# Performance work log

Hardware: AMD Instinct MI355X
Metric: run time of the kernel (lower is better)

Reference implementation:

```python
import jax, jax.numpy as jnp
import numpy as np

N_NODES = 50000
N_EDGES = 800000
IN_DIM = 128
OUT_DIM = 64
NEG_SLOPE = 0.01  # torch F.leaky_relu default


def setup_inputs() -> dict:
    key = jax.random.key(0)
    ks = jax.random.split(key, 7)
    h = jax.random.normal(ks[0], (N_NODES, IN_DIM), dtype=jnp.float32)
    embed = jax.random.uniform(ks[1], (N_EDGES, 1), dtype=jnp.float32)
    src = jax.random.randint(ks[2], (N_EDGES,), 0, N_NODES)
    dst = jax.random.randint(ks[3], (N_EDGES,), 0, N_NODES)
    # parameters (Linear weights, no bias); stored as [in, out] for x @ W
    W_fc = jax.random.normal(ks[4], (IN_DIM, OUT_DIM), dtype=jnp.float32) / np.sqrt(IN_DIM)
    W_attn = jax.random.normal(ks[5], (3 * OUT_DIM, 1), dtype=jnp.float32) / np.sqrt(3 * OUT_DIM)
    W_feat = jax.random.normal(ks[6], (1, OUT_DIM), dtype=jnp.float32)
    return {"h": h, "embed": embed, "src": src, "dst": dst,
            "W_fc": W_fc, "W_attn": W_attn, "W_feat": W_feat}


def reference(h, embed, src, dst, W_fc, W_attn, W_feat):
    n = h.shape[0]
    z = h @ W_fc                                  # [N, D]
    # split attn weight so we never materialize the [E, 3D] concat
    Wa_src, Wa_dst, Wa_feat = jnp.split(W_attn, 3, axis=0)  # each [D, 1]
    a_src = (z @ Wa_src)[:, 0]                    # [N]
    a_dst = (z @ Wa_dst)[:, 0]                    # [N]
    dfeat = embed @ W_feat                        # [E, D]
    e = a_src[src] + a_dst[dst] + (dfeat @ Wa_feat)[:, 0]  # [E]
    e = jnp.where(e >= 0, e, NEG_SLOPE * e)       # leaky_relu
    # segment softmax over incoming edges of each dst node
    seg_max = jax.ops.segment_max(e, dst, num_segments=n)  # [N]
    ex = jnp.exp(e - seg_max[dst])                # [E]
    denom = jax.ops.segment_sum(ex, dst, num_segments=n)   # [N]
    alpha = ex / denom[dst]                       # [E]
    # weighted scatter-sum of source features
    out = jax.ops.segment_sum(alpha[:, None] * z[src], dst, num_segments=n)  # [N, D]
    return out
```

## Files before the change

### kernel.cpp

```cpp
#include <hip/hip_runtime.h>
#include <hip/hip_fp16.h>

#define N_NODES 50000
#define N_EDGES 800000
#define IN_DIM 128
#define OUT_DIM 64
#define NEG_SLOPE 0.01f

#define BUCK_SHIFT 6
#define BUCK_NODES 64
#define NBUCK ((N_NODES + BUCK_NODES - 1) / BUCK_NODES)
#define CAP 1536
#define EPB 3136
#define NBLK_SCAT ((N_EDGES + EPB - 1) / EPB)

typedef unsigned int uint;

__device__ __forceinline__ uint f2h(float x) {
    return (uint)__half_as_ushort(__float2half_rn(x));
}
__device__ __forceinline__ float h2f(unsigned short u) {
    return __half2float(__ushort_as_half(u));
}

__launch_bounds__(256)
__global__ void k_fc(const float* __restrict__ h,
                     const float* __restrict__ W_fc,
                     const float* __restrict__ W_attn,
                     const float* __restrict__ W_feat,
                     uint* __restrict__ z16, float* __restrict__ a_src, float* __restrict__ a_dst,
                     int* __restrict__ gcursor, float* __restrict__ c_ws) {
    __shared__ float Wlds[IN_DIM * OUT_DIM];
    const float4* Wg = (const float4*)W_fc;
    float4* Wl = (float4*)Wlds;
    #pragma unroll
    for (int i = 0; i < 8; ++i) Wl[threadIdx.x + i * 256] = Wg[threadIdx.x + i * 256];

    int g = blockIdx.x * 256 + threadIdx.x;
    if (g < NBUCK) gcursor[g] = g * CAP;
    if (blockIdx.x == 0 && threadIdx.x < 64) {
        int lane = threadIdx.x;
        float p = W_feat[lane] * W_attn[128 + lane];
        #pragma unroll
        for (int off = 32; off; off >>= 1) p += __shfl_xor(p, off, 64);
        if (lane == 0) c_ws[0] = p;
    }
    __syncthreads();

    int quad = g >> 4;
    int og   = g & 15;
    int n0 = quad * 4;
    if (n0 >= N_NODES) return;

    bool valid[4];
    const float4* hrow[4];
    #pragma unroll
    for (int i = 0; i < 4; ++i) {
        int n = n0 + i;
        valid[i] = (n < N_NODES);
        hrow[i] = (const float4*)(h + (size_t)(valid[i] ? n : (N_NODES - 1)) * IN_DIM);
    }

    float acc[4][4];
    #pragma unroll
    for (int i = 0; i < 4; ++i)
        #pragma unroll
        for (int d = 0; d < 4; ++d) acc[i][d] = 0.f;

    for (int kc = 0; kc < IN_DIM / 4; ++kc) {
        float4 hv[4];
        #pragma unroll
        for (int i = 0; i < 4; ++i) hv[i] = hrow[i][kc];
        #pragma unroll
        for (int j = 0; j < 4; ++j) {
            float4 wv = *(const float4*)(Wlds + (size_t)(kc * 4 + j) * OUT_DIM + og * 4);
            #pragma unroll
            for (int i = 0; i < 4; ++i) {
                float hh = (j == 0) ? hv[i].x : (j == 1) ? hv[i].y : (j == 2) ? hv[i].z : hv[i].w;
                acc[i][0] += hh * wv.x;
                acc[i][1] += hh * wv.y;
                acc[i][2] += hh * wv.z;
                acc[i][3] += hh * wv.w;
            }
        }
    }

    #pragma unroll
    for (int i = 0; i < 4; ++i) {
        if (!valid[i]) continue;
        uint* zr = z16 + (size_t)(n0 + i) * (OUT_DIM / 2) + og * 2;
        zr[0] = f2h(acc[i][0]) | (f2h(acc[i][1]) << 16);
        zr[1] = f2h(acc[i][2]) | (f2h(acc[i][3]) << 16);
    }

    float was0 = W_attn[og * 4], was1 = W_attn[og * 4 + 1],
          was2 = W_attn[og * 4 + 2], was3 = W_attn[og * 4 + 3];
    float wad0 = W_attn[64 + og * 4], wad1 = W_attn[64 + og * 4 + 1],
          wad2 = W_attn[64 + og * 4 + 2], wad3 = W_attn[64 + og * 4 + 3];
    #pragma unroll
    for (int i = 0; i < 4; ++i) {
        float ps = acc[i][0] * was0 + acc[i][1] * was1 + acc[i][2] * was2 + acc[i][3] * was3;
        float pd = acc[i][0] * wad0 + acc[i][1] * wad1 + acc[i][2] * wad2 + acc[i][3] * wad3;
        ps += __shfl_xor(ps, 1, 64); ps += __shfl_xor(ps, 2, 64);
        ps += __shfl_xor(ps, 4, 64); ps += __shfl_xor(ps, 8, 64);
        pd += __shfl_xor(pd, 1, 64); pd += __shfl_xor(pd, 2, 64);
        pd += __shfl_xor(pd, 4, 64); pd += __shfl_xor(pd, 8, 64);
        if (og == 0 && valid[i]) { a_src[n0 + i] = ps; a_dst[n0 + i] = pd; }
    }
}

__launch_bounds__(1024)
__global__ void k_binscat(const int* __restrict__ src, const int* __restrict__ dst,
                          const float* __restrict__ embed,
                          const float* __restrict__ a_src,
                          const float* __restrict__ c_ws,
                          int* __restrict__ gcursor, uint2* __restrict__ entries) {
    __shared__ int hist[NBUCK];
    __shared__ int boff[NBUCK];
    int t = threadIdx.x;
    if (t < NBUCK) hist[t] = 0;
    __syncthreads();

    int e0 = blockIdx.x * EPB;
    int e1 = e0 + EPB; if (e1 > N_EDGES) e1 = N_EDGES;
    int m = e1 - e0;
    float cc = c_ws[0];

    uint keyr[4]; float valr[4];
    bool own[4] = {false, false, false, false};

    int i0 = t * 4;
    if (i0 + 3 < m) {
        int4   s4 = ((const int4*)(src + e0))[t];
        int4   d4 = ((const int4*)(dst + e0))[t];
        float4 m4 = ((const float4*)(embed + e0))[t];
        int    ss[4] = {s4.x, s4.y, s4.z, s4.w};
        int    dd[4] = {d4.x, d4.y, d4.z, d4.w};
        float  mm[4] = {m4.x, m4.y, m4.z, m4.w};
        #pragma unroll
        for (int u = 0; u < 4; ++u) {
            uint b = (uint)dd[u] >> BUCK_SHIFT, dl = (uint)dd[u] & (BUCK_NODES - 1);
            keyr[u] = (uint)ss[u] | (dl << 16) | (b << 22);
            valr[u] = a_src[ss[u]] + cc * mm[u];
            own[u] = true;
            atomicAdd(&hist[b], 1);
        }
    } else {
        #pragma unroll
        for (int u = 0; u < 4; ++u) {
            int i = i0 + u;
            if (i < m) {
                int e = e0 + i;
                int s = src[e], d = dst[e];
                uint b = (uint)d >> BUCK_SHIFT, dl = (uint)d & (BUCK_NODES - 1);
                keyr[u] = (uint)s | (dl << 16) | (b << 22);
                valr[u] = a_src[s] + cc * embed[e];
                own[u] = true;
                atomicAdd(&hist[b], 1);
            }
        }
    }
    __syncthreads();

    if (t < NBUCK) {
        int c = hist[t];
        boff[t] = c ? atomicAdd(&gcursor[t], c) : 0;
        hist[t] = 0;
    }
    __syncthreads();

    #pragma unroll
    for (int u = 0; u < 4; ++u) {
        if (!own[u]) continue;
        uint b = keyr[u] >> 22;
        int pos = boff[b] + atomicAdd(&hist[b], 1);
        entries[pos] = make_uint2(keyr[u] & 0x3FFFFFu, __float_as_uint(valr[u]));
    }
}

__launch_bounds__(1024)
__global__ void k_gather(const int* __restrict__ gcursor, const uint2* __restrict__ entries,
                         const float* __restrict__ a_dst,
                         const uint* __restrict__ z16, float* __restrict__ out) {
    __shared__ uint2 s_stash[CAP];
    __shared__ uint  s_pk2[CAP];
    __shared__ float s_adst[BUCK_NODES];
    __shared__ int hist[BUCK_NODES], hoff[BUCK_NODES], hcur[BUCK_NODES];

    int b = blockIdx.x;
    int t = threadIdx.x, lane = t & 63, wid = t >> 6;
    int base = b * CAP;
    int m = gcursor[b] - base;
    if (m > CAP) m = CAP;

    if (t < BUCK_NODES) {
        hist[t] = 0;
        int n = b * BUCK_NODES + t;
        s_adst[t] = (n < N_NODES) ? a_dst[n] : 0.f;
    }
    __syncthreads();

    for (int i = t; i < m; i += 1024) {
        uint2 p = entries[base + i];
        s_stash[i] = p;
        atomicAdd(&hist[(p.x >> 16) & 63], 1);
    }
    __syncthreads();

    if (wid == 0) {
        int v = hist[lane], sc = v;
        #pragma unroll
        for (int off = 1; off < 64; off <<= 1) {
            int u = __shfl_up(sc, off, 64);
            if (lane >= off) sc += u;
        }
        hoff[lane] = sc - v;
        hcur[lane] = sc - v;
    }
    __syncthreads();

    for (int i = t; i < m; i += 1024) {
        uint2 p = s_stash[i];
        int dl = (p.x >> 16) & 63;
        float ev = __uint_as_float(p.y) + s_adst[dl];
        ev = (ev >= 0.f) ? ev : NEG_SLOPE * ev;
        float ex = __expf(ev);
        int pos = atomicAdd(&hcur[dl], 1);
        s_pk2[pos] = (p.x & 0xFFFFu) | (f2h(ex) << 16);
    }
    __syncthreads();

    int half = lane >> 5, dp = lane & 31;
    for (int k = 0; k < 4; ++k) {
        int dl = wid * 4 + k;
        int n = b * BUCK_NODES + dl;
        if (n >= N_NODES) continue;
        int j0 = hoff[dl], c = hist[dl], j1 = j0 + c;
        float accx = 0.f, accy = 0.f, den = 0.f;
        for (int j = j0; j < j1; j += 8) {
            uint pk[4];
            #pragma unroll
            for (int u = 0; u < 4; ++u) {
                int idx = j + 4 * half + u;
                int idc = (idx < j1) ? idx : (j1 - 1);
                pk[u] = s_pk2[idc];
                if (idx >= j1) pk[u] &= 0xFFFFu;
            }
            uint zv[4];
            #pragma unroll
            for (int u = 0; u < 4; ++u) zv[u] = z16[(size_t)(pk[u] & 0xFFFFu) * 32 + dp];
            #pragma unroll
            for (int u = 0; u < 4; ++u) {
                float ex = h2f((unsigned short)(pk[u] >> 16));
                den  += ex;
                accx += ex * h2f((unsigned short)(zv[u] & 0xFFFFu));
                accy += ex * h2f((unsigned short)(zv[u] >> 16));
            }
        }
        accx += __shfl_xor(accx, 32, 64);
        accy += __shfl_xor(accy, 32, 64);
        den  += __shfl_xor(den, 32, 64);
        if (lane < 32) {
            float2 r = (c > 0) ? make_float2(accx / den, accy / den) : make_float2(0.f, 0.f);
            ((float2*)(out + (size_t)n * OUT_DIM))[dp] = r;
        }
    }
}

extern "C" void kernel_launch(void* const* d_in, const int* in_sizes, int n_in,
                              void* d_out, int out_size, void* d_ws, size_t ws_size,
                              hipStream_t stream) {
    const float* h      = (const float*)d_in[0];
    const float* embed  = (const float*)d_in[1];
    const int*   src    = (const int*)d_in[2];
    const int*   dst    = (const int*)d_in[3];
    const float* W_fc   = (const float*)d_in[4];
    const float* W_attn = (const float*)d_in[5];
    const float* W_feat = (const float*)d_in[6];

    float* ws      = (float*)d_ws;
    uint*  z16     = (uint*)ws;
    uint2* entries = (uint2*)(z16 + (size_t)N_NODES * 32);
    float* a_src   = (float*)(entries + (size_t)NBUCK * CAP);
    float* a_dst   = a_src + N_NODES;
    float* c_ws    = a_dst + N_NODES;
    int*   gcursor = (int*)(c_ws + 1);

    float* out = (float*)d_out;

    k_fc<<<(N_NODES * 4 + 255) / 256, 256, 0, stream>>>(h, W_fc, W_attn, W_feat,
                                                        z16, a_src, a_dst, gcursor, c_ws);
    k_binscat<<<NBLK_SCAT, 1024, 0, stream>>>(src, dst, embed, a_src, c_ws,
                                              gcursor, entries);
    k_gather<<<NBUCK, 1024, 0, stream>>>(gcursor, entries, a_dst, z16, out);
}
```

Before: 68.85 us.

## Merge FC and edge binning into one kernel, defer a_src lookup to gather

Combines the node linear-transform kernel and the edge bucketing kernel into a single launch, with blocks split by index between the two roles, so both run at the same time instead of one after the other. The a_src gather is moved out of the binning phase and into the gather kernel, which removes the data dependency between the two roles. The bucket cursors are now zeroed with a memset and store relative offsets. FC blocks now use 1024 threads each, which may change occupancy. The gather kernel does an extra random read of a_src for each edge.

```diff
diff --git a/kernel.cpp b/kernel.cpp
--- a/kernel.cpp
+++ b/kernel.cpp
@@ -13,6 +13,8 @@
 #define CAP 1536
 #define EPB 3136
 #define NBLK_SCAT ((N_EDGES + EPB - 1) / EPB)
+#define NBLK_FC   ((N_NODES * 4 + 1023) / 1024)
+#define NBLK_PREP (NBLK_SCAT + NBLK_FC)
 
 typedef unsigned int uint;
 
@@ -23,164 +25,161 @@
     return __half2float(__ushort_as_half(u));
 }
 
-__launch_bounds__(256)
-__global__ void k_fc(const float* __restrict__ h,
-                     const float* __restrict__ W_fc,
-                     const float* __restrict__ W_attn,
-                     const float* __restrict__ W_feat,
-                     uint* __restrict__ z16, float* __restrict__ a_src, float* __restrict__ a_dst,
-                     int* __restrict__ gcursor, float* __restrict__ c_ws) {
+__launch_bounds__(1024)
+__global__ void k_prep(const float* __restrict__ h,
+                       const float* __restrict__ W_fc,
+                       const float* __restrict__ W_attn,
+                       const float* __restrict__ W_feat,
+                       const int* __restrict__ src, const int* __restrict__ dst,
+                       const float* __restrict__ embed,
+                       uint* __restrict__ z16, float* __restrict__ a_src, float* __restrict__ a_dst,
+                       int* __restrict__ gcursor, uint2* __restrict__ entries) {
     __shared__ float Wlds[IN_DIM * OUT_DIM];
-    const float4* Wg = (const float4*)W_fc;
-    float4* Wl = (float4*)Wlds;
-    #pragma unroll
-    for (int i = 0; i < 8; ++i) Wl[threadIdx.x + i * 256] = Wg[threadIdx.x + i * 256];
-
-    int g = blockIdx.x * 256 + threadIdx.x;
-    if (g < NBUCK) gcursor[g] = g * CAP;
-    if (blockIdx.x == 0 && threadIdx.x < 64) {
-        int lane = threadIdx.x;
-        float p = W_feat[lane] * W_attn[128 + lane];
-        #pragma unroll
-        for (int off = 32; off; off >>= 1) p += __shfl_xor(p, off, 64);
-        if (lane == 0) c_ws[0] = p;
-    }
-    __syncthreads();
-
-    int quad = g >> 4;
-    int og   = g & 15;
-    int n0 = quad * 4;
-    if (n0 >= N_NODES) return;
-
-    bool valid[4];
-    const float4* hrow[4];
-    #pragma unroll
-    for (int i = 0; i < 4; ++i) {
-        int n = n0 + i;
-        valid[i] = (n < N_NODES);
-        hrow[i] = (const float4*)(h + (size_t)(valid[i] ? n : (N_NODES - 1)) * IN_DIM);
-    }
-
-    float acc[4][4];
-    #pragma unroll
-    for (int i = 0; i < 4; ++i)
-        #pragma unroll
-        for (int d = 0; d < 4; ++d) acc[i][d] = 0.f;
-
-    for (int kc = 0; kc < IN_DIM / 4; ++kc) {
-        float4 hv[4];
-        #pragma unroll
-        for (int i = 0; i < 4; ++i) hv[i] = hrow[i][kc];
-        #pragma unroll
-        for (int j = 0; j < 4; ++j) {
-            float4 wv = *(const float4*)(Wlds + (size_t)(kc * 4 + j) * OUT_DIM + og * 4);
-            #pragma unroll
-            for (int i = 0; i < 4; ++i) {
-                float hh = (j == 0) ? hv[i].x : (j == 1) ? hv[i].y : (j == 2) ? hv[i].z : hv[i].w;
-                acc[i][0] += hh * wv.x;
-                acc[i][1] += hh * wv.y;
-                acc[i][2] += hh * wv.z;
-                acc[i][3] += hh * wv.w;
-            }
-        }
-    }
-
-    #pragma unroll
-    for (int i = 0; i < 4; ++i) {
-        if (!valid[i]) continue;
-        uint* zr = z16 + (size_t)(n0 + i) * (OUT_DIM / 2) + og * 2;
-        zr[0] = f2h(acc[i][0]) | (f2h(acc[i][1]) << 16);
-        zr[1] = f2h(acc[i][2]) | (f2h(acc[i][3]) << 16);
-    }
-
-    float was0 = W_attn[og * 4], was1 = W_attn[og * 4 + 1],
-          was2 = W_attn[og * 4 + 2], was3 = W_attn[og * 4 + 3];
-    float wad0 = W_attn[64 + og * 4], wad1 = W_attn[64 + og * 4 + 1],
-          wad2 = W_attn[64 + og * 4 + 2], wad3 = W_attn[64 + og * 4 + 3];
-    #pragma unroll
-    for (int i = 0; i < 4; ++i) {
-        float ps = acc[i][0] * was0 + acc[i][1] * was1 + acc[i][2] * was2 + acc[i][3] * was3;
-        float pd = acc[i][0] * wad0 + acc[i][1] * wad1 + acc[i][2] * wad2 + acc[i][3] * wad3;
-        ps += __shfl_xor(ps, 1, 64); ps += __shfl_xor(ps, 2, 64);
-        ps += __shfl_xor(ps, 4, 64); ps += __shfl_xor(ps, 8, 64);
-        pd += __shfl_xor(pd, 1, 64); pd += __shfl_xor(pd, 2, 64);
-        pd += __shfl_xor(pd, 4, 64); pd += __shfl_xor(pd, 8, 64);
-        if (og == 0 && valid[i]) { a_src[n0 + i] = ps; a_dst[n0 + i] = pd; }
-    }
-}
-
-__launch_bounds__(1024)
-__global__ void k_binscat(const int* __restrict__ src, const int* __restrict__ dst,
-                          const float* __restrict__ embed,
-                          const float* __restrict__ a_src,
-                          const float* __restrict__ c_ws,
-                          int* __restrict__ gcursor, uint2* __restrict__ entries) {
     __shared__ int hist[NBUCK];
     __shared__ int boff[NBUCK];
+    __shared__ float s_c;
+
     int t = threadIdx.x;
-    if (t < NBUCK) hist[t] = 0;
-    __syncthreads();
-
-    int e0 = blockIdx.x * EPB;
-    int e1 = e0 + EPB; if (e1 > N_EDGES) e1 = N_EDGES;
-    int m = e1 - e0;
-    float cc = c_ws[0];
-
-    uint keyr[4]; float valr[4];
-    bool own[4] = {false, false, false, false};
-
-    int i0 = t * 4;
-    if (i0 + 3 < m) {
-        int4   s4 = ((const int4*)(src + e0))[t];
-        int4   d4 = ((const int4*)(dst + e0))[t];
-        float4 m4 = ((const float4*)(embed + e0))[t];
-        int    ss[4] = {s4.x, s4.y, s4.z, s4.w};
-        int    dd[4] = {d4.x, d4.y, d4.z, d4.w};
-        float  mm[4] = {m4.x, m4.y, m4.z, m4.w};
-        #pragma unroll
-        for (int u = 0; u < 4; ++u) {
-            uint b = (uint)dd[u] >> BUCK_SHIFT, dl = (uint)dd[u] & (BUCK_NODES - 1);
-            keyr[u] = (uint)ss[u] | (dl << 16) | (b << 22);
-            valr[u] = a_src[ss[u]] + cc * mm[u];
-            own[u] = true;
-            atomicAdd(&hist[b], 1);
-        }
-    } else {
-        #pragma unroll
-        for (int u = 0; u < 4; ++u) {
-            int i = i0 + u;
-            if (i < m) {
-                int e = e0 + i;
-                int s = src[e], d = dst[e];
-                uint b = (uint)d >> BUCK_SHIFT, dl = (uint)d & (BUCK_NODES - 1);
-                keyr[u] = (uint)s | (dl << 16) | (b << 22);
-                valr[u] = a_src[s] + cc * embed[e];
+
+    if (blockIdx.x < NBLK_SCAT) {
+        if (t < 64) {
+            float p = W_feat[t] * W_attn[128 + t];
+            #pragma unroll
+            for (int off = 32; off; off >>= 1) p += __shfl_xor(p, off, 64);
+            if (t == 0) s_c = p;
+        }
+        if (t < NBUCK) hist[t] = 0;
+        __syncthreads();
+        float cc = s_c;
+
+        int e0 = blockIdx.x * EPB;
+        int e1 = e0 + EPB; if (e1 > N_EDGES) e1 = N_EDGES;
+        int m = e1 - e0;
+
+        uint keyr[4]; float valr[4];
+        bool own[4] = {false, false, false, false};
+
+        int i0 = t * 4;
+        if (i0 + 3 < m) {
+            int4   s4 = ((const int4*)(src + e0))[t];
+            int4   d4 = ((const int4*)(dst + e0))[t];
+            float4 m4 = ((const float4*)(embed + e0))[t];
+            int    ss[4] = {s4.x, s4.y, s4.z, s4.w};
+            int    dd[4] = {d4.x, d4.y, d4.z, d4.w};
+            float  mm[4] = {m4.x, m4.y, m4.z, m4.w};
+            #pragma unroll
+            for (int u = 0; u < 4; ++u) {
+                uint b = (uint)dd[u] >> BUCK_SHIFT, dl = (uint)dd[u] & (BUCK_NODES - 1);
+                keyr[u] = (uint)ss[u] | (dl << 16) | (b << 22);
+                valr[u] = cc * mm[u];
                 own[u] = true;
                 atomicAdd(&hist[b], 1);
             }
-        }
-    }
-    __syncthreads();
-
-    if (t < NBUCK) {
-        int c = hist[t];
-        boff[t] = c ? atomicAdd(&gcursor[t], c) : 0;
-        hist[t] = 0;
-    }
-    __syncthreads();
-
-    #pragma unroll
-    for (int u = 0; u < 4; ++u) {
-        if (!own[u]) continue;
-        uint b = keyr[u] >> 22;
-        int pos = boff[b] + atomicAdd(&hist[b], 1);
-        entries[pos] = make_uint2(keyr[u] & 0x3FFFFFu, __float_as_uint(valr[u]));
+        } else {
+            #pragma unroll
+            for (int u = 0; u < 4; ++u) {
+                int i = i0 + u;
+                if (i < m) {
+                    int e = e0 + i;
+                    int s = src[e], d = dst[e];
+                    uint b = (uint)d >> BUCK_SHIFT, dl = (uint)d & (BUCK_NODES - 1);
+                    keyr[u] = (uint)s | (dl << 16) | (b << 22);
+                    valr[u] = cc * embed[e];
+                    own[u] = true;
+                    atomicAdd(&hist[b], 1);
+                }
+            }
+        }
+        __syncthreads();
+
+        if (t < NBUCK) {
+            int c = hist[t];
+            boff[t] = c ? atomicAdd(&gcursor[t], c) : 0;
+            hist[t] = 0;
+        }
+        __syncthreads();
+
+        #pragma unroll
+        for (int u = 0; u < 4; ++u) {
+            if (!own[u]) continue;
+            uint b = keyr[u] >> 22;
+            int pos = (int)(b * CAP) + boff[b] + atomicAdd(&hist[b], 1);
+            entries[pos] = make_uint2(keyr[u] & 0x3FFFFFu, __float_as_uint(valr[u]));
+        }
+    } else {
+        const float4* Wg = (const float4*)W_fc;
+        float4* Wl = (float4*)Wlds;
+        #pragma unroll
+        for (int i = 0; i < 2; ++i) Wl[t + i * 1024] = Wg[t + i * 1024];
+        __syncthreads();
+
+        int g = (blockIdx.x - NBLK_SCAT) * 1024 + t;
+        int quad = g >> 4;
+        int og   = g & 15;
+        int n0 = quad * 4;
+        if (n0 >= N_NODES) return;
+
+        bool valid[4];
+        const float4* hrow[4];
+        #pragma unroll
+        for (int i = 0; i < 4; ++i) {
+            int n = n0 + i;
+            valid[i] = (n < N_NODES);
+            hrow[i] = (const float4*)(h + (size_t)(valid[i] ? n : (N_NODES - 1)) * IN_DIM);
+        }
+
+        float acc[4][4];
+        #pragma unroll
+        for (int i = 0; i < 4; ++i)
+            #pragma unroll
+            for (int d = 0; d < 4; ++d) acc[i][d] = 0.f;
+
+        for (int kc = 0; kc < IN_DIM / 4; ++kc) {
+            float4 hv[4];
+            #pragma unroll
+            for (int i = 0; i < 4; ++i) hv[i] = hrow[i][kc];
+            #pragma unroll
+            for (int j = 0; j < 4; ++j) {
+                float4 wv = *(const float4*)(Wlds + (size_t)(kc * 4 + j) * OUT_DIM + og * 4);
+                #pragma unroll
+                for (int i = 0; i < 4; ++i) {
+                    float hh = (j == 0) ? hv[i].x : (j == 1) ? hv[i].y : (j == 2) ? hv[i].z : hv[i].w;
+                    acc[i][0] += hh * wv.x;
+                    acc[i][1] += hh * wv.y;
+                    acc[i][2] += hh * wv.z;
+                    acc[i][3] += hh * wv.w;
+                }
+            }
+        }
+
+        #pragma unroll
+        for (int i = 0; i < 4; ++i) {
+            if (!valid[i]) continue;
+            uint* zr = z16 + (size_t)(n0 + i) * (OUT_DIM / 2) + og * 2;
+            zr[0] = f2h(acc[i][0]) | (f2h(acc[i][1]) << 16);
+            zr[1] = f2h(acc[i][2]) | (f2h(acc[i][3]) << 16);
+        }
+
+        float was0 = W_attn[og * 4], was1 = W_attn[og * 4 + 1],
+              was2 = W_attn[og * 4 + 2], was3 = W_attn[og * 4 + 3];
+        float wad0 = W_attn[64 + og * 4], wad1 = W_attn[64 + og * 4 + 1],
+              wad2 = W_attn[64 + og * 4 + 2], wad3 = W_attn[64 + og * 4 + 3];
+        #pragma unroll
+        for (int i = 0; i < 4; ++i) {
+            float ps = acc[i][0] * was0 + acc[i][1] * was1 + acc[i][2] * was2 + acc[i][3] * was3;
+            float pd = acc[i][0] * wad0 + acc[i][1] * wad1 + acc[i][2] * wad2 + acc[i][3] * wad3;
+            ps += __shfl_xor(ps, 1, 64); ps += __shfl_xor(ps, 2, 64);
+            ps += __shfl_xor(ps, 4, 64); ps += __shfl_xor(ps, 8, 64);
+            pd += __shfl_xor(pd, 1, 64); pd += __shfl_xor(pd, 2, 64);
+            pd += __shfl_xor(pd, 4, 64); pd += __shfl_xor(pd, 8, 64);
+            if (og == 0 && valid[i]) { a_src[n0 + i] = ps; a_dst[n0 + i] = pd; }
+        }
     }
 }
 
 __launch_bounds__(1024)
 __global__ void k_gather(const int* __restrict__ gcursor, const uint2* __restrict__ entries,
-                         const float* __restrict__ a_dst,
+                         const float* __restrict__ a_src, const float* __restrict__ a_dst,
                          const uint* __restrict__ z16, float* __restrict__ out) {
     __shared__ uint2 s_stash[CAP];
     __shared__ uint  s_pk2[CAP];
@@ -190,7 +189,7 @@
     int b = blockIdx.x;
     int t = threadIdx.x, lane = t & 63, wid = t >> 6;
     int base = b * CAP;
-    int m = gcursor[b] - base;
+    int m = gcursor[b];
     if (m > CAP) m = CAP;
 
     if (t < BUCK_NODES) {
@@ -202,6 +201,7 @@
 
     for (int i = t; i < m; i += 1024) {
         uint2 p = entries[base + i];
+        p.y = __float_as_uint(__uint_as_float(p.y) + a_src[p.x & 0xFFFFu]);
         s_stash[i] = p;
         atomicAdd(&hist[(p.x >> 16) & 63], 1);
     }
@@ -283,14 +283,12 @@
     uint2* entries = (uint2*)(z16 + (size_t)N_NODES * 32);
     float* a_src   = (float*)(entries + (size_t)NBUCK * CAP);
     float* a_dst   = a_src + N_NODES;
-    float* c_ws    = a_dst + N_NODES;
-    int*   gcursor = (int*)(c_ws + 1);
+    int*   gcursor = (int*)(a_dst + N_NODES);
 
     float* out = (float*)d_out;
 
-    k_fc<<<(N_NODES * 4 + 255) / 256, 256, 0, stream>>>(h, W_fc, W_attn, W_feat,
-                                                        z16, a_src, a_dst, gcursor, c_ws);
-    k_binscat<<<NBLK_SCAT, 1024, 0, stream>>>(src, dst, embed, a_src, c_ws,
-                                              gcursor, entries);
-    k_gather<<<NBUCK, 1024, 0, stream>>>(gcursor, entries, a_dst, z16, out);
-}
+    hipMemsetAsync(gcursor, 0, NBUCK * sizeof(int), stream);
+    k_prep<<<NBLK_PREP, 1024, 0, stream>>>(h, W_fc, W_attn, W_feat, src, dst, embed,
+                                           z16, a_src, a_dst, gcursor, entries);
+    k_gather<<<NBUCK, 1024, 0, stream>>>(gcursor, entries, a_src, a_dst, z16, out);
+}
```

Result: slower. 72.30 us (+5.0%).
